# Kernel tuning notes

Hardware: AMD Instinct MI355X
Metric: run time of the kernel (lower is better)

Reference implementation:

```python
import jax, jax.numpy as jnp
import numpy as np

N_HEAD = 8


def setup_inputs() -> dict:
    key = jax.random.key(0)
    ks = jax.random.split(key, 5)
    D = 512
    q = jax.random.normal(ks[0], (2, 4096, D), dtype=jnp.float32)
    s = 0.02  # init scale for weights
    Wq = jax.random.normal(ks[1], (D, D), dtype=jnp.float32) * s
    Wk = jax.random.normal(ks[2], (D, D), dtype=jnp.float32) * s
    Wv = jax.random.normal(ks[3], (D, D), dtype=jnp.float32) * s
    Wo = jax.random.normal(ks[4], (D, D), dtype=jnp.float32) * s
    z = jnp.zeros((D,), dtype=jnp.float32)
    return {"q": q, "Wq": Wq, "bq": z, "Wk": Wk, "bk": z, "Wv": Wv, "bv": z, "Wo": Wo, "bo": z}


def _split_heads(x, n_head):
    # (b, s, c) -> (b, h, s, c//h)
    b, s, c = x.shape
    return x.reshape(b, s, n_head, c // n_head).transpose(0, 2, 1, 3)


def reference(q, Wq, bq, Wk, bk, Wv, bv, Wo, bo):
    # Linear projections (nn.Linear: x @ W.T + b); self-attention (kv = q)
    qp = _split_heads(q @ Wq.T + bq, N_HEAD)  # (b, h, s, dh)
    kp = _split_heads(q @ Wk.T + bk, N_HEAD)
    vp = _split_heads(q @ Wv.T + bv, N_HEAD)
    dh = qp.shape[-1]
    scale = 1.0 / jnp.sqrt(jnp.asarray(dh, dtype=qp.dtype))
    # unfused MATH-backend SDPA: full [b,h,s,s] scores, stable softmax, no dropout (eval)
    scores = jnp.einsum("bhqd,bhkd->bhqk", qp, kp) * scale
    probs = jax.nn.softmax(scores, axis=-1)
    attn = jnp.einsum("bhqk,bhkd->bhqd", probs, vp)  # (b, h, s, dh)
    # merge heads: (b, h, s, dh) -> (b, s, h*dh)
    b, h, s, _ = attn.shape
    merged = attn.transpose(0, 2, 1, 3).reshape(b, s, h * dh)
    return merged @ Wo.T + bo
```

## Files before the change

### kernel.cpp

```cpp
#include <hip/hip_runtime.h>
#include <hip/hip_bf16.h>
#include <math.h>

typedef __attribute__((ext_vector_type(8))) short bf16x8;
typedef __attribute__((ext_vector_type(4))) short bf16x4;
typedef __attribute__((ext_vector_type(4))) float f32x4;

__device__ __forceinline__ unsigned short f2bf(float f) {
    union { float f; unsigned int u; } v; v.f = f;
    unsigned int u = v.u;
    u += 0x7fffu + ((u >> 16) & 1u);
    return (unsigned short)(u >> 16);
}

__device__ __forceinline__ f32x4 mfma16(bf16x4 a, bf16x4 b, f32x4 c) {
#if __has_builtin(__builtin_amdgcn_mfma_f32_16x16x16bf16_1k)
    return __builtin_amdgcn_mfma_f32_16x16x16bf16_1k(a, b, c, 0, 0, 0);
#else
    asm volatile("v_mfma_f32_16x16x16_bf16 %0, %1, %2, %0\n\ts_nop 7"
                 : "+v"(c) : "v"(a), "v"(b));
    return c;
#endif
}

__device__ __forceinline__ unsigned packbf2(float a, float b) {
    __hip_bfloat162 h = __float22bfloat162_rn(float2{a, b});
    union { __hip_bfloat162 h; unsigned u; } v; v.h = h;
    return v.u;
}

__device__ __forceinline__ float fmax3(float a, float b, float c) {
    return fmaxf(fmaxf(a, b), c);
}

template<int A_BF16>
__device__ __forceinline__ void gemm_body(const void* Ap, const float* W,
                                          f32x4 (&acc)[4][4],
                                          unsigned short (*As)[40], unsigned short (*Bs)[40],
                                          int bm, int bn, int t)
{
    constexpr int Kdim = 512;
    const int lane = t & 63, g = lane >> 4, c = lane & 15;
    const int w = t >> 6, wr = w >> 1, wc = w & 1;

    uint4  paB[2];
    float4 paF[4];
    float4 pw[4];
    const int ccB = (t & 3) * 8, r0B = t >> 2;
    const int c4  = (t & 7) * 4, r0F = t >> 3;

    if (A_BF16) {
        const unsigned short* A = (const unsigned short*)Ap;
        for (int p = 0; p < 2; ++p)
            paB[p] = *(const uint4*)(A + (size_t)(bm + r0B + p * 64) * Kdim + ccB);
    } else {
        const float* A = (const float*)Ap;
        for (int p = 0; p < 4; ++p)
            paF[p] = *(const float4*)(A + (size_t)(bm + r0F + p * 32) * Kdim + c4);
    }
    for (int p = 0; p < 4; ++p)
        pw[p] = *(const float4*)(W + (size_t)(bn + r0F + p * 32) * Kdim + c4);

    for (int k0 = 0; k0 < Kdim; k0 += 32) {
        __syncthreads();
        if (A_BF16) {
            for (int p = 0; p < 2; ++p)
                *(uint4*)&As[r0B + p * 64][ccB] = paB[p];
        } else {
            for (int p = 0; p < 4; ++p) {
                float4 v = paF[p];
                ushort4 hv;
                hv.x = f2bf(v.x); hv.y = f2bf(v.y); hv.z = f2bf(v.z); hv.w = f2bf(v.w);
                *(ushort4*)&As[r0F + p * 32][c4] = hv;
            }
        }
        for (int p = 0; p < 4; ++p) {
            float4 v = pw[p];
            ushort4 hv;
            hv.x = f2bf(v.x); hv.y = f2bf(v.y); hv.z = f2bf(v.z); hv.w = f2bf(v.w);
            *(ushort4*)&Bs[r0F + p * 32][c4] = hv;
        }
        __syncthreads();
        if (k0 + 32 < Kdim) {
            const int kn = k0 + 32;
            if (A_BF16) {
                const unsigned short* A = (const unsigned short*)Ap;
                for (int p = 0; p < 2; ++p)
                    paB[p] = *(const uint4*)(A + (size_t)(bm + r0B + p * 64) * Kdim + kn + ccB);
            } else {
                const float* A = (const float*)Ap;
                for (int p = 0; p < 4; ++p)
                    paF[p] = *(const float4*)(A + (size_t)(bm + r0F + p * 32) * Kdim + kn + c4);
            }
            for (int p = 0; p < 4; ++p)
                pw[p] = *(const float4*)(W + (size_t)(bn + r0F + p * 32) * Kdim + kn + c4);
        }
        bf16x8 af[4], bfr[4];
        for (int i = 0; i < 4; ++i)
            af[i] = *(const bf16x8*)&As[wr * 64 + i * 16 + c][g * 8];
        for (int j = 0; j < 4; ++j)
            bfr[j] = *(const bf16x8*)&Bs[wc * 64 + j * 16 + c][g * 8];
        for (int i = 0; i < 4; ++i)
            for (int j = 0; j < 4; ++j)
                acc[i][j] = __builtin_amdgcn_mfma_f32_16x16x32_bf16(af[i], bfr[j], acc[i][j], 0, 0, 0);
    }
}

__global__ __launch_bounds__(256, 2)
void gemm_qkv(const float* __restrict__ q,
              const float* __restrict__ Wq, const float* __restrict__ bq,
              const float* __restrict__ Wk, const float* __restrict__ bk,
              const float* __restrict__ Wv, const float* __restrict__ bv,
              unsigned short* __restrict__ Qo, unsigned short* __restrict__ Ko,
              unsigned short* __restrict__ Vo)
{
    __shared__ unsigned short As[128][40];
    __shared__ unsigned short Bs[128][40];
    const int t = threadIdx.x, z = blockIdx.z;
    const int lane = t & 63, g = lane >> 4, c = lane & 15;
    const int w = t >> 6, wr = w >> 1, wc = w & 1;
    const int bm = blockIdx.x * 128, bn = blockIdx.y * 128;

    const float* W    = (z == 0) ? Wq : (z == 1) ? Wk : Wv;
    const float* bias = (z == 0) ? bq : (z == 1) ? bk : bv;
    unsigned short* Out = (z == 0) ? Qo : (z == 1) ? Ko : Vo;
    const float osc = (z == 0) ? 0.125f * 1.44269504f : 1.0f;

    f32x4 acc[4][4] = {};
    gemm_body<0>((const void*)q, W, acc, As, Bs, bm, bn, t);

    float bv4[4];
    for (int j = 0; j < 4; ++j) bv4[j] = bias[bn + wc * 64 + j * 16 + c];
    for (int i = 0; i < 4; ++i)
        for (int j = 0; j < 4; ++j)
            for (int r = 0; r < 4; ++r) {
                int m = bm + wr * 64 + i * 16 + 4 * g + r;
                int n = bn + wc * 64 + j * 16 + c;
                float val = (acc[i][j][r] + bv4[j]) * osc;
                int b = m >> 12, s = m & 4095, h = n >> 6, d = n & 63;
                if (z < 2)
                    Out[((((size_t)b * 8 + h) * 4096 + s) << 6) + d] = f2bf(val);
                else
                    Out[(((size_t)b * 8 + h) * 64 + d) * 4096 + s] = f2bf(val);
            }
}

__global__ __launch_bounds__(256, 2)
void gemm_out(const unsigned short* __restrict__ A, const float* __restrict__ W,
              const float* __restrict__ bias, float* __restrict__ Out)
{
    __shared__ unsigned short As[128][40];
    __shared__ unsigned short Bs[128][40];
    const int t = threadIdx.x;
    const int lane = t & 63, g = lane >> 4, c = lane & 15;
    const int w = t >> 6, wr = w >> 1, wc = w & 1;
    const int bm = blockIdx.x * 128, bn = blockIdx.y * 128;

    f32x4 acc[4][4] = {};
    gemm_body<1>((const void*)A, W, acc, As, Bs, bm, bn, t);

    float bv4[4];
    for (int j = 0; j < 4; ++j) bv4[j] = bias[bn + wc * 64 + j * 16 + c];
    for (int i = 0; i < 4; ++i)
        for (int j = 0; j < 4; ++j)
            for (int r = 0; r < 4; ++r) {
                int m = bm + wr * 64 + i * 16 + 4 * g + r;
                int n = bn + wc * 64 + j * 16 + c;
                Out[(size_t)m * 512 + n] = acc[i][j][r] + bv4[j];
            }
}

__global__ __launch_bounds__(512, 4)
void attn128(const unsigned short* __restrict__ Q, const unsigned short* __restrict__ Kh,
             const unsigned short* __restrict__ VT, unsigned short* __restrict__ Mo)
{
    __shared__ unsigned short Ks[2 * 64 * 64];
    __shared__ unsigned short Vs[2 * 64 * 64];

    const int t = threadIdx.x, w = t >> 6, lane = t & 63, g = lane >> 4, c = lane & 15;
    const int idp = (blockIdx.x & 7) * 64 + (blockIdx.x >> 3);
    const int bh = idp >> 5;
    const int q0 = (idp & 31) * 128;
    const unsigned short* Qb = Q + (size_t)bh * 4096 * 64;
    const unsigned short* Kb = Kh + (size_t)bh * 4096 * 64;
    const unsigned short* Vb = VT + (size_t)bh * 64 * 4096;

    bf16x8 qf0, qf1;
    {
        int qr = q0 + w * 16 + c;
        qf0 = *(const bf16x8*)(Qb + (size_t)qr * 64 + g * 8);
        qf1 = *(const bf16x8*)(Qb + (size_t)qr * 64 + 32 + g * 8);
    }

    f32x4 o[4] = {};
    f32x4 lacc = {};
    float nm = 0.f;

    bf16x4 ones;
    ones[0] = ones[1] = ones[2] = ones[3] = (short)0x3F80;

    const int srow = t >> 3, s0 = t & 7;
    const int scol = s0 * 8;
    const int woff = srow * 64 + ((s0 ^ (srow & 7)) << 3);
    const unsigned short* kp0 = Kb + (size_t)srow * 64 + scol;
    const unsigned short* vp0 = Vb + (size_t)srow * 4096 + scol;

    uint4 ka = *(const uint4*)(kp0);
    uint4 va = *(const uint4*)(vp0);
    *(uint4*)&Ks[woff] = ka;
    *(uint4*)&Vs[woff] = va;

    const float THR = 10.f;
    const int c7 = c & 7;

    auto tile_iter = [&](int jt, const unsigned short* Kc, const unsigned short* Vc,
                         unsigned short* Kn, unsigned short* Vn) {
        __syncthreads();
        if (jt < 63) {
            ka = *(const uint4*)(kp0 + (size_t)(jt + 1) * 4096);
            va = *(const uint4*)(vp0 + (jt + 1) * 64);
        }

        f32x4 ta[4];
        #pragma unroll
        for (int nt = 0; nt < 4; ++nt) {
            int row = nt * 16 + c;
            bf16x8 kf0 = *(const bf16x8*)&Kc[row * 64 + ((g ^ c7) << 3)];
            bf16x8 kf1 = *(const bf16x8*)&Kc[row * 64 + (((4 + g) ^ c7) << 3)];
            f32x4 z = {nm, nm, nm, nm};
            z = __builtin_amdgcn_mfma_f32_16x16x32_bf16(kf0, qf0, z, 0, 0, 0);
            z = __builtin_amdgcn_mfma_f32_16x16x32_bf16(kf1, qf1, z, 0, 0, 0);
            ta[nt] = z;
        }

        float tm = fmax3(fmax3(fmax3(ta[0][0], ta[0][1], ta[0][2]),
                               fmax3(ta[0][3], ta[1][0], ta[1][1]),
                               fmax3(ta[1][2], ta[1][3], ta[2][0])),
                         fmax3(ta[2][1], ta[2][2], ta[2][3]),
                         fmax3(fmax3(ta[3][0], ta[3][1], ta[3][2]), ta[3][3], ta[3][3]));
        if (!__all(tm <= THR)) {
            float pm = tm;
            pm = fmaxf(pm, __shfl_xor(pm, 16));
            pm = fmaxf(pm, __shfl_xor(pm, 32));
            float dm = fmaxf(pm, 0.f);
            nm -= dm;
            float al = exp2f(-dm);
            #pragma unroll
            for (int nt = 0; nt < 4; ++nt)
                #pragma unroll
                for (int r = 0; r < 4; ++r) ta[nt][r] -= dm;
            #pragma unroll
            for (int r = 0; r < 4; ++r) {
                float ar = __shfl(al, 4 * g + r);
                #pragma unroll
                for (int nd = 0; nd < 4; ++nd) o[nd][r] *= ar;
                lacc[r] *= ar;
            }
        }

        bf16x4 pf[4];
        #pragma unroll
        for (int nt = 0; nt < 4; ++nt) {
            union { unsigned u[2]; bf16x4 v; } pk;
            pk.u[0] = packbf2(exp2f(ta[nt][0]), exp2f(ta[nt][1]));
            pk.u[1] = packbf2(exp2f(ta[nt][2]), exp2f(ta[nt][3]));
            pf[nt] = pk.v;
        }

        #pragma unroll
        for (int nd = 0; nd < 4; ++nd) {
            int row = nd * 16 + c;
            #pragma unroll
            for (int nt = 0; nt < 4; ++nt) {
                int off = row * 64 + (((2 * nt + (g >> 1)) ^ c7) << 3) + ((g & 1) << 2);
                bf16x4 vf = *(const bf16x4*)&Vc[off];
                o[nd] = mfma16(pf[nt], vf, o[nd]);
            }
        }
        #pragma unroll
        for (int nt = 0; nt < 4; ++nt)
            lacc = mfma16(pf[nt], ones, lacc);

        if (jt < 63) {
            *(uint4*)&Kn[woff] = ka;
            *(uint4*)&Vn[woff] = va;
        }
    };

    for (int jt2 = 0; jt2 < 64; jt2 += 2) {
        tile_iter(jt2,     &Ks[0],    &Vs[0],    &Ks[4096], &Vs[4096]);
        tile_iter(jt2 + 1, &Ks[4096], &Vs[4096], &Ks[0],    &Vs[0]);
    }

    const int b = bh >> 3, h = bh & 7;
    #pragma unroll
    for (int r = 0; r < 4; ++r) {
        float inv = 1.f / lacc[r];
        int m = b * 4096 + q0 + w * 16 + 4 * g + r;
        #pragma unroll
        for (int nd = 0; nd < 4; ++nd) {
            int n = h * 64 + nd * 16 + c;
            Mo[(size_t)m * 512 + n] = f2bf(o[nd][r] * inv);
        }
    }
}

extern "C" void kernel_launch(void* const* d_in, const int* in_sizes, int n_in,
                              void* d_out, int out_size, void* d_ws, size_t ws_size,
                              hipStream_t stream) {
    const float* q  = (const float*)d_in[0];
    const float* Wq = (const float*)d_in[1];
    const float* bq = (const float*)d_in[2];
    const float* Wk = (const float*)d_in[3];
    const float* bk = (const float*)d_in[4];
    const float* Wv = (const float*)d_in[5];
    const float* bv = (const float*)d_in[6];
    const float* Wo = (const float*)d_in[7];
    const float* bo = (const float*)d_in[8];

    unsigned short* Qb = (unsigned short*)d_ws;
    unsigned short* Kb = Qb + (size_t)16 * 4096 * 64;
    unsigned short* Vt = Kb + (size_t)16 * 4096 * 64;
    unsigned short* Mg = Vt + (size_t)16 * 4096 * 64;

    dim3 gb(256);
    dim3 gqkv(64, 4, 3);
    gemm_qkv<<<gqkv, gb, 0, stream>>>(q, Wq, bq, Wk, bk, Wv, bv, Qb, Kb, Vt);

    dim3 ga(512), gba(512);
    attn128<<<ga, gba, 0, stream>>>(Qb, Kb, Vt, Mg);

    dim3 gg(64, 4);
    gemm_out<<<gg, gb, 0, stream>>>(Mg, Wo, bo, (float*)d_out);
}
```

Before: 181.9 us.

## Process 128-key K/V tiles per barrier and raise wave priority around MFMAs

Doubles the K/V shared-memory tile to 128 keys per stage, so each stage runs two 64-key softmax/PV halves between barriers and prefetches twice as much global data per sync. This halves the number of __syncthreads and load/store rounds. It also wraps the MFMA phases in s_setprio to favour matrix issue. The larger LDS footprint (64KB per block) may reduce resident blocks per CU and increases register pressure from the extra prefetch registers.

```diff
diff --git a/kernel.cpp b/kernel.cpp
--- a/kernel.cpp
+++ b/kernel.cpp
@@ -174,8 +174,8 @@
 void attn128(const unsigned short* __restrict__ Q, const unsigned short* __restrict__ Kh,
              const unsigned short* __restrict__ VT, unsigned short* __restrict__ Mo)
 {
-    __shared__ unsigned short Ks[2 * 64 * 64];
-    __shared__ unsigned short Vs[2 * 64 * 64];
+    __shared__ unsigned short Ks[2 * 128 * 64];
+    __shared__ unsigned short Vs[2 * 64 * 128];
 
     const int t = threadIdx.x, w = t >> 6, lane = t & 63, g = lane >> 4, c = lane & 15;
     const int idp = (blockIdx.x & 7) * 64 + (blockIdx.x >> 3);
@@ -200,28 +200,29 @@
     ones[0] = ones[1] = ones[2] = ones[3] = (short)0x3F80;
 
     const int srow = t >> 3, s0 = t & 7;
-    const int scol = s0 * 8;
-    const int woff = srow * 64 + ((s0 ^ (srow & 7)) << 3);
-    const unsigned short* kp0 = Kb + (size_t)srow * 64 + scol;
-    const unsigned short* vp0 = Vb + (size_t)srow * 4096 + scol;
-
-    uint4 ka = *(const uint4*)(kp0);
-    uint4 va = *(const uint4*)(vp0);
-    *(uint4*)&Ks[woff] = ka;
-    *(uint4*)&Vs[woff] = va;
+    const int scol = s0 * 8, r7 = srow & 7;
+    const int woffK  = srow * 64 + ((s0 ^ r7) << 3);
+    const int woffKB = (64 + srow) * 64 + ((s0 ^ r7) << 3);
+    const int woffV  = srow * 128 + ((s0 ^ r7) << 3);
+    const int woffVB = srow * 128 + ((8 + (s0 ^ r7)) << 3);
+    const unsigned short* kpA = Kb + (size_t)srow * 64 + scol;
+    const unsigned short* vpA = Vb + (size_t)srow * 4096 + scol;
+
+    uint4 kaA = *(const uint4*)(kpA);
+    uint4 kaB = *(const uint4*)(kpA + 64 * 64);
+    uint4 vaA = *(const uint4*)(vpA);
+    uint4 vaB = *(const uint4*)(vpA + 64);
+    *(uint4*)&Ks[woffK]  = kaA;
+    *(uint4*)&Ks[woffKB] = kaB;
+    *(uint4*)&Vs[woffV]  = vaA;
+    *(uint4*)&Vs[woffVB] = vaB;
 
     const float THR = 10.f;
     const int c7 = c & 7;
 
-    auto tile_iter = [&](int jt, const unsigned short* Kc, const unsigned short* Vc,
-                         unsigned short* Kn, unsigned short* Vn) {
-        __syncthreads();
-        if (jt < 63) {
-            ka = *(const uint4*)(kp0 + (size_t)(jt + 1) * 4096);
-            va = *(const uint4*)(vp0 + (jt + 1) * 64);
-        }
-
+    auto half_iter = [&](const unsigned short* Kc, const unsigned short* Vc, int h8) {
         f32x4 ta[4];
+        __builtin_amdgcn_s_setprio(1);
         #pragma unroll
         for (int nt = 0; nt < 4; ++nt) {
             int row = nt * 16 + c;
@@ -232,6 +233,7 @@
             z = __builtin_amdgcn_mfma_f32_16x16x32_bf16(kf1, qf1, z, 0, 0, 0);
             ta[nt] = z;
         }
+        __builtin_amdgcn_s_setprio(0);
 
         float tm = fmax3(fmax3(fmax3(ta[0][0], ta[0][1], ta[0][2]),
                                fmax3(ta[0][3], ta[1][0], ta[1][1]),
@@ -267,12 +269,13 @@
             pf[nt] = pk.v;
         }
 
+        __builtin_amdgcn_s_setprio(1);
         #pragma unroll
         for (int nd = 0; nd < 4; ++nd) {
             int row = nd * 16 + c;
             #pragma unroll
             for (int nt = 0; nt < 4; ++nt) {
-                int off = row * 64 + (((2 * nt + (g >> 1)) ^ c7) << 3) + ((g & 1) << 2);
+                int off = row * 128 + ((h8 + ((2 * nt + (g >> 1)) ^ c7)) << 3) + ((g & 1) << 2);
                 bf16x4 vf = *(const bf16x4*)&Vc[off];
                 o[nd] = mfma16(pf[nt], vf, o[nd]);
             }
@@ -280,16 +283,33 @@
         #pragma unroll
         for (int nt = 0; nt < 4; ++nt)
             lacc = mfma16(pf[nt], ones, lacc);
-
-        if (jt < 63) {
-            *(uint4*)&Kn[woff] = ka;
-            *(uint4*)&Vn[woff] = va;
-        }
+        __builtin_amdgcn_s_setprio(0);
     };
 
-    for (int jt2 = 0; jt2 < 64; jt2 += 2) {
-        tile_iter(jt2,     &Ks[0],    &Vs[0],    &Ks[4096], &Vs[4096]);
-        tile_iter(jt2 + 1, &Ks[4096], &Vs[4096], &Ks[0],    &Vs[0]);
+    auto tile_iter = [&](int it, const unsigned short* Kc, const unsigned short* Vc,
+                         unsigned short* Kn, unsigned short* Vn) {
+        __syncthreads();
+        if (it < 31) {
+            const unsigned short* kp = kpA + (size_t)(it + 1) * 8192;
+            const unsigned short* vp = vpA + (it + 1) * 128;
+            kaA = *(const uint4*)(kp);
+            kaB = *(const uint4*)(kp + 64 * 64);
+            vaA = *(const uint4*)(vp);
+            vaB = *(const uint4*)(vp + 64);
+        }
+        half_iter(Kc, Vc, 0);
+        half_iter(Kc + 64 * 64, Vc, 8);
+        if (it < 31) {
+            *(uint4*)&Kn[woffK]  = kaA;
+            *(uint4*)&Kn[woffKB] = kaB;
+            *(uint4*)&Vn[woffV]  = vaA;
+            *(uint4*)&Vn[woffVB] = vaB;
+        }
+    };
+
+    for (int it2 = 0; it2 < 32; it2 += 2) {
+        tile_iter(it2,     &Ks[0],    &Vs[0],    &Ks[8192], &Vs[8192]);
+        tile_iter(it2 + 1, &Ks[8192], &Vs[8192], &Ks[0],    &Vs[0]);
     }
 
     const int b = bh >> 3, h = bh & 7;
```

Measured after the change: 174.4 us. 1.04x faster.
